# Kernel tuning notes

Hardware: AMD Instinct MI355X
Metric: run time of the kernel (lower is better)

The kernel has to match this reference:

```python
import jax, jax.numpy as jnp
import numpy as np

H = 100  # hidden size
EPS = 1e-5  # BatchNorm1d default eps


def setup_inputs() -> dict:
    key = jax.random.key(0)
    ks = jax.random.split(key, 9)
    s_ih = 1.0 / np.sqrt(H)
    inp = {
        "x": jax.random.normal(ks[0], (16, 4096, 40), dtype=jnp.float32),
        "W_ih": jax.random.uniform(ks[1], (4 * H, 40), jnp.float32, -s_ih, s_ih),
        "W_hh": jax.random.uniform(ks[2], (4 * H, H), jnp.float32, -s_ih, s_ih),
        "b_ih": jax.random.uniform(ks[3], (4 * H,), jnp.float32, -s_ih, s_ih),
        "b_hh": jax.random.uniform(ks[4], (4 * H,), jnp.float32, -s_ih, s_ih),
        "W1": jax.random.uniform(ks[5], (H, H), jnp.float32, -s_ih, s_ih),
        "b1": jax.random.uniform(ks[6], (H,), jnp.float32, -s_ih, s_ih),
        "gamma": jnp.ones((H,), jnp.float32),
        "beta": jnp.zeros((H,), jnp.float32),
        "W2": jax.random.uniform(ks[7], (40, H), jnp.float32, -s_ih, s_ih),
        "b2": jax.random.uniform(ks[8], (40,), jnp.float32, -s_ih, s_ih),
    }
    return inp


def _lstm_last_h(x, W_ih, W_hh, b_ih, b_hh):
    # x: [B, T, 40] -> precompute input projections for all timesteps
    B = x.shape[0]
    xg = jnp.einsum("bti,gi->tbg", x, W_ih) + b_ih + b_hh  # [T, B, 4H]
    W_hh_T = W_hh.T  # [H, 4H]

    def step(carry, xg_t):
        h, c = carry
        z = xg_t + h @ W_hh_T  # [B, 4H]
        i = jax.nn.sigmoid(z[:, 0 * H:1 * H])
        f = jax.nn.sigmoid(z[:, 1 * H:2 * H])
        g = jnp.tanh(z[:, 2 * H:3 * H])
        o = jax.nn.sigmoid(z[:, 3 * H:4 * H])
        c = f * c + i * g
        h = o * jnp.tanh(c)
        return (h, c), None

    h0 = jnp.zeros((B, H), x.dtype)
    c0 = jnp.zeros((B, H), x.dtype)
    (h_T, _), _ = jax.lax.scan(step, (h0, c0), xg)
    return h_T  # [B, H] == out[:, -1, :]


def reference(x, W_ih, W_hh, b_ih, b_hh, W1, b1, gamma, beta, W2, b2):
    h = _lstm_last_h(x, W_ih, W_hh, b_ih, b_hh)  # [B, H]
    y = h @ W1.T + b1  # Linear(100, 100)
    # BatchNorm1d in training mode: batch statistics, biased variance
    mu = jnp.mean(y, axis=0)
    var = jnp.mean((y - mu) ** 2, axis=0)
    y = (y - mu) * jax.lax.rsqrt(var + EPS) * gamma + beta
    y = y @ W2.T + b2  # Linear(100, 40)
    return y.reshape(-1, 10, 4)
```

## Files before the change

kernel.cpp:

```cpp
#include <hip/hip_runtime.h>
#include <cstddef>
#include <cstdint>

#define H100  100
#define G4    400
#define BATCH 16
#define TTOT  4096
#define NIN   40

__device__ __forceinline__ float fast_rcp(float x) { return __builtin_amdgcn_rcpf(x); }

__device__ __forceinline__ float gate_act(float z, bool is_g) {
    float m = is_g ? -2.0f : -1.0f;
    float e = __expf(m * z);
    float r = fast_rcp(1.0f + e);
    return is_g ? (2.0f * r - 1.0f) : r;
}
__device__ __forceinline__ float tanh_fast(float x) {
    float e = __expf(-2.0f * x);
    float r = fast_rcp(1.0f + e);
    return 2.0f * r - 1.0f;
}

__global__ __launch_bounds__(256) void xg_kernel(
    const float* __restrict__ x, const float* __restrict__ W_ih,
    const float* __restrict__ b_ih, const float* __restrict__ b_hh,
    float* __restrict__ xg, int t0, int steps, int chunkT)
{
    __shared__ float W_lds[NIN * G4];
    __shared__ float x_lds[16 * NIN];
    __shared__ float bias_lds[G4];

    int tid = threadIdx.x;
    int blocks_per_b = (steps + 15) >> 4;
    int b   = blockIdx.x / blocks_per_b;
    int tt  = blockIdx.x % blocks_per_b;
    int lt0 = tt * 16;
    int ntau = min(16, steps - lt0);

    for (int p = tid; p < NIN * G4; p += 256) {
        int g = p / NIN, i = p % NIN;
        W_lds[i * G4 + g] = W_ih[p];
    }
    for (int p = tid; p < G4; p += 256) bias_lds[p] = b_ih[p] + b_hh[p];
    const float* xsrc = x + ((size_t)b * TTOT + (size_t)(t0 + lt0)) * NIN;
    for (int p = tid; p < ntau * NIN; p += 256) x_lds[p] = xsrc[p];
    __syncthreads();

    int ntask = ntau * G4;
    for (int p = tid; p < ntask; p += 256) {
        int tau = p / G4, g = p % G4;
        float acc = bias_lds[g];
        #pragma unroll
        for (int i = 0; i < NIN; i++)
            acc = fmaf(x_lds[tau * NIN + i], W_lds[i * G4 + g], acc);
        xg[((size_t)b * chunkT + (size_t)(lt0 + tau)) * G4 + g] = acc;
    }
}

using h2_t = decltype(__builtin_amdgcn_cvt_pkrtz(0.0f, 0.0f));

__device__ __forceinline__ int h2i(h2_t v) { int r; __builtin_memcpy(&r, &v, 4); return r; }
__device__ __forceinline__ h2_t i2h(int v) { h2_t r; __builtin_memcpy(&r, &v, 4); return r; }

#if __has_builtin(__builtin_amdgcn_fdot2)
__device__ __forceinline__ float fdot2(h2_t a, h2_t b, float c) {
    return __builtin_amdgcn_fdot2(a, b, c, false);
}
#else
__device__ __forceinline__ float fdot2(h2_t a, h2_t b, float c) {
    float d;
    asm("v_dot2_f32_f16 %0, %1, %2, %3" : "=v"(d) : "v"(a), "v"(b), "v"(c));
    return d;
}
#endif

#define PIN1(a) asm volatile("" : "+v"(a))

__global__ __launch_bounds__(256)
__attribute__((amdgpu_waves_per_eu(1, 1)))
void lstm_kernel(
    const float* __restrict__ xg, const float* __restrict__ W_hh,
    float* __restrict__ hc, int t0, int steps, int chunkT)
{
    __shared__ float a_lds[2][G4];

    const int x = threadIdx.x;
    const int b = blockIdx.x;
    const int l = x & 63;
    const bool hasB = (x < G4 - 256);
    const int  rA = x;
    const int  rB = hasB ? (x + 256) : 0;

    const float2* wra2 = (const float2*)(W_hh + (size_t)rA * H100);
    const float2* wrb2 = (const float2*)(W_hh + (size_t)rB * H100);
#define LDW(q) \
    int wa##q = h2i(__builtin_amdgcn_cvt_pkrtz(wra2[q].x, wra2[q].y)); \
    int wb##q = h2i(__builtin_amdgcn_cvt_pkrtz(wrb2[q].x, wrb2[q].y)); \
    PIN1(wa##q); PIN1(wb##q);
    LDW(0)  LDW(1)  LDW(2)  LDW(3)  LDW(4)  LDW(5)  LDW(6)  LDW(7)
    LDW(8)  LDW(9)  LDW(10) LDW(11) LDW(12) LDW(13) LDW(14) LDW(15)
    LDW(16) LDW(17) LDW(18) LDW(19) LDW(20) LDW(21) LDW(22) LDW(23)
    LDW(24) LDW(25) LDW(26) LDW(27) LDW(28) LDW(29) LDW(30) LDW(31)
    LDW(32) LDW(33) LDW(34) LDW(35) LDW(36) LDW(37) LDW(38) LDW(39)
    LDW(40) LDW(41) LDW(42) LDW(43) LDW(44) LDW(45) LDW(46) LDW(47)
    LDW(48) LDW(49)
#undef LDW

    float* hch = hc;
    float* hcc = hc + BATCH * H100;

    float h0 = 0.f, h1 = 0.f, c0 = 0.f, c1 = 0.f;
    int hpi = 0;
    if (l < 50) {
        if (t0 != 0) {
            float2 hv = ((const float2*)(hch + b * H100))[l];
            float2 cv = ((const float2*)(hcc + b * H100))[l];
            h0 = hv.x; h1 = hv.y; c0 = cv.x; c1 = cv.y;
        }
        hpi = h2i(__builtin_amdgcn_cvt_pkrtz(h0, h1));
    }

    const float* xgb = xg + (size_t)b * chunkT * G4;
    float xcA = xgb[rA];
    float xcB = hasB ? xgb[rB] : 0.0f;

    const bool is_gA = (x >= 200) && (x < 300);
    const bool is_gB = (x < 44);

#define RLH2(src, idx) i2h(__builtin_amdgcn_readlane((src), (idx)))
#define DOTQ(q, aA, aB) { const h2_t u = RLH2(hpi, q); \
    aA = fdot2(i2h(wa##q), u, aA); \
    aB = fdot2(i2h(wb##q), u, aB); }

    #pragma unroll 1
    for (int t = 0; t < steps; t++) {
        float nxA = 0.f, nxB = 0.f;
        if (t + 1 < steps) {
            const float* p = xgb + (size_t)(t + 1) * G4;
            nxA = p[rA];
            nxB = p[rB];
        }

        float aA0 = 0, aA1 = 0, aB0 = 0, aB1 = 0;
        DOTQ(0,  aA0, aB0) DOTQ(1,  aA1, aB1) DOTQ(2,  aA0, aB0) DOTQ(3,  aA1, aB1)
        DOTQ(4,  aA0, aB0) DOTQ(5,  aA1, aB1) DOTQ(6,  aA0, aB0) DOTQ(7,  aA1, aB1)
        DOTQ(8,  aA0, aB0) DOTQ(9,  aA1, aB1) DOTQ(10, aA0, aB0) DOTQ(11, aA1, aB1)
        DOTQ(12, aA0, aB0) DOTQ(13, aA1, aB1) DOTQ(14, aA0, aB0) DOTQ(15, aA1, aB1)
        DOTQ(16, aA0, aB0) DOTQ(17, aA1, aB1) DOTQ(18, aA0, aB0) DOTQ(19, aA1, aB1)
        DOTQ(20, aA0, aB0) DOTQ(21, aA1, aB1) DOTQ(22, aA0, aB0) DOTQ(23, aA1, aB1)
        DOTQ(24, aA0, aB0) DOTQ(25, aA1, aB1) DOTQ(26, aA0, aB0) DOTQ(27, aA1, aB1)
        DOTQ(28, aA0, aB0) DOTQ(29, aA1, aB1) DOTQ(30, aA0, aB0) DOTQ(31, aA1, aB1)
        DOTQ(32, aA0, aB0) DOTQ(33, aA1, aB1) DOTQ(34, aA0, aB0) DOTQ(35, aA1, aB1)
        DOTQ(36, aA0, aB0) DOTQ(37, aA1, aB1) DOTQ(38, aA0, aB0) DOTQ(39, aA1, aB1)
        DOTQ(40, aA0, aB0) DOTQ(41, aA1, aB1) DOTQ(42, aA0, aB0) DOTQ(43, aA1, aB1)
        DOTQ(44, aA0, aB0) DOTQ(45, aA1, aB1) DOTQ(46, aA0, aB0) DOTQ(47, aA1, aB1)
        DOTQ(48, aA0, aB0) DOTQ(49, aA1, aB1)

        float zA = xcA + (aA0 + aA1);
        float zB = xcB + (aB0 + aB1);

        const int par = t & 1;
        a_lds[par][rA] = gate_act(zA, is_gA);
        if (hasB) a_lds[par][x + 256] = gate_act(zB, is_gB);
        asm volatile("s_waitcnt lgkmcnt(0)" ::: "memory");
        __builtin_amdgcn_s_barrier();

        if (l < 50) {
            const float* ab = a_lds[par];
            float2 gi = ((const float2*)(ab))[l];
            float2 gf = ((const float2*)(ab + 100))[l];
            float2 gg = ((const float2*)(ab + 200))[l];
            float2 go = ((const float2*)(ab + 300))[l];
            c0 = fmaf(gf.x, c0, gi.x * gg.x);
            c1 = fmaf(gf.y, c1, gi.y * gg.y);
            h0 = go.x * tanh_fast(c0);
            h1 = go.y * tanh_fast(c1);
            hpi = h2i(__builtin_amdgcn_cvt_pkrtz(h0, h1));
        }
        xcA = nxA; xcB = nxB;
    }

    if (x < 64 && l < 50) {
        ((float2*)(hch + b * H100))[l] = make_float2(h0, h1);
        ((float2*)(hcc + b * H100))[l] = make_float2(c0, c1);
    }
#undef DOTQ
#undef RLH2
}

__global__ __launch_bounds__(256) void head_kernel(
    const float* __restrict__ hc, const float* __restrict__ W1,
    const float* __restrict__ b1, const float* __restrict__ gamma,
    const float* __restrict__ beta, const float* __restrict__ W2,
    const float* __restrict__ b2, float* __restrict__ out)
{
    __shared__ float h_s[BATCH * H100];
    __shared__ float W1_s[H100 * 101];
    __shared__ float y1_s[BATCH * H100];
    __shared__ float W2_s[40 * 101];
    __shared__ float scale_s[H100], shift_s[H100];

    int tid = threadIdx.x;
    for (int p = tid; p < BATCH * H100; p += 256) h_s[p] = hc[p];
    for (int p = tid; p < H100 * H100; p += 256)
        W1_s[(p / H100) * 101 + p % H100] = W1[p];
    for (int p = tid; p < 40 * H100; p += 256)
        W2_s[(p / H100) * 101 + p % H100] = W2[p];
    __syncthreads();

    for (int p = tid; p < BATCH * H100; p += 256) {
        int b = p / H100, j = p % H100;
        float acc = b1[j];
        for (int k = 0; k < H100; k++)
            acc = fmaf(h_s[b * H100 + k], W1_s[j * 101 + k], acc);
        y1_s[b * H100 + j] = acc;
    }
    __syncthreads();

    if (tid < H100) {
        float mu = 0.0f;
        for (int b = 0; b < BATCH; b++) mu += y1_s[b * H100 + tid];
        mu *= (1.0f / BATCH);
        float var = 0.0f;
        for (int b = 0; b < BATCH; b++) {
            float d = y1_s[b * H100 + tid] - mu;
            var = fmaf(d, d, var);
        }
        var *= (1.0f / BATCH);
        float sc = gamma[tid] * rsqrtf(var + 1e-5f);
        scale_s[tid] = sc;
        shift_s[tid] = beta[tid] - mu * sc;
    }
    __syncthreads();

    for (int p = tid; p < BATCH * 40; p += 256) {
        int b = p / 40, o = p % 40;
        float acc = b2[o];
        for (int k = 0; k < H100; k++)
            acc = fmaf(fmaf(y1_s[b * H100 + k], scale_s[k], shift_s[k]),
                       W2_s[o * 101 + k], acc);
        out[p] = acc;
    }
}

extern "C" void kernel_launch(void* const* d_in, const int* in_sizes, int n_in,
                              void* d_out, int out_size, void* d_ws, size_t ws_size,
                              hipStream_t stream)
{
    const float* x     = (const float*)d_in[0];
    const float* W_ih  = (const float*)d_in[1];
    const float* W_hh  = (const float*)d_in[2];
    const float* b_ih  = (const float*)d_in[3];
    const float* b_hh  = (const float*)d_in[4];
    const float* W1    = (const float*)d_in[5];
    const float* b1    = (const float*)d_in[6];
    const float* gamma = (const float*)d_in[7];
    const float* beta  = (const float*)d_in[8];
    const float* W2    = (const float*)d_in[9];
    const float* b2    = (const float*)d_in[10];
    float* out = (float*)d_out;

    float* hc = (float*)d_ws;
    float* xg = (float*)((char*)d_ws + 16384);
    size_t avail    = ws_size > 16384 ? ws_size - 16384 : 0;
    size_t per_step = (size_t)BATCH * G4 * sizeof(float);
    size_t ct       = (avail / per_step) & ~(size_t)15;
    int chunkT = ct > TTOT ? TTOT : (int)ct;
    if (chunkT < 16) chunkT = 16;

    for (int t0 = 0; t0 < TTOT; t0 += chunkT) {
        int steps = (TTOT - t0 < chunkT) ? (TTOT - t0) : chunkT;
        int bpb = (steps + 15) / 16;
        xg_kernel<<<dim3(BATCH * bpb), 256, 0, stream>>>(
            x, W_ih, b_ih, b_hh, xg, t0, steps, chunkT);
        lstm_kernel<<<dim3(BATCH), 256, 0, stream>>>(
            xg, W_hh, hc, t0, steps, chunkT);
    }
    head_kernel<<<1, 256, 0, stream>>>(hc, W1, b1, gamma, beta, W2, b2, out);
}
```

Before: 2.727 ms.

## Store precomputed input projections in fp16 and enlarge xg time tile

The precomputed input-gate projections are now written and read as half precision, halving workspace traffic and letting larger chunks fit in the workspace, so fewer kernel launches may be needed. The xg kernel's time tile grows from 16 to 128 steps, so the W_ih transpose into LDS is amortised over more timesteps at the cost of fewer blocks. The recurrent kernel converts the halves back to float. The risk is precision loss in the gate pre-activations accumulated over 4096 steps, while the serial recurrence likely still dominates runtime.

```diff
diff --git a/kernel.cpp b/kernel.cpp
--- a/kernel.cpp
+++ b/kernel.cpp
@@ -1,4 +1,5 @@
 #include <hip/hip_runtime.h>
+#include <hip/hip_fp16.h>
 #include <cstddef>
 #include <cstdint>
 
@@ -7,6 +8,7 @@
 #define BATCH 16
 #define TTOT  4096
 #define NIN   40
+#define TAU   128
 
 __device__ __forceinline__ float fast_rcp(float x) { return __builtin_amdgcn_rcpf(x); }
 
@@ -25,18 +27,18 @@
 __global__ __launch_bounds__(256) void xg_kernel(
     const float* __restrict__ x, const float* __restrict__ W_ih,
     const float* __restrict__ b_ih, const float* __restrict__ b_hh,
-    float* __restrict__ xg, int t0, int steps, int chunkT)
+    __half* __restrict__ xg, int t0, int steps, int chunkT)
 {
     __shared__ float W_lds[NIN * G4];
-    __shared__ float x_lds[16 * NIN];
+    __shared__ float x_lds[TAU * NIN];
     __shared__ float bias_lds[G4];
 
     int tid = threadIdx.x;
-    int blocks_per_b = (steps + 15) >> 4;
+    int blocks_per_b = (steps + TAU - 1) / TAU;
     int b   = blockIdx.x / blocks_per_b;
     int tt  = blockIdx.x % blocks_per_b;
-    int lt0 = tt * 16;
-    int ntau = min(16, steps - lt0);
+    int lt0 = tt * TAU;
+    int ntau = min(TAU, steps - lt0);
 
     for (int p = tid; p < NIN * G4; p += 256) {
         int g = p / NIN, i = p % NIN;
@@ -54,7 +56,7 @@
         #pragma unroll
         for (int i = 0; i < NIN; i++)
             acc = fmaf(x_lds[tau * NIN + i], W_lds[i * G4 + g], acc);
-        xg[((size_t)b * chunkT + (size_t)(lt0 + tau)) * G4 + g] = acc;
+        xg[((size_t)b * chunkT + (size_t)(lt0 + tau)) * G4 + g] = __float2half(acc);
     }
 }
 
@@ -80,7 +82,7 @@
 __global__ __launch_bounds__(256)
 __attribute__((amdgpu_waves_per_eu(1, 1)))
 void lstm_kernel(
-    const float* __restrict__ xg, const float* __restrict__ W_hh,
+    const __half* __restrict__ xg, const float* __restrict__ W_hh,
     float* __restrict__ hc, int t0, int steps, int chunkT)
 {
     __shared__ float a_lds[2][G4];
@@ -121,9 +123,9 @@
         hpi = h2i(__builtin_amdgcn_cvt_pkrtz(h0, h1));
     }
 
-    const float* xgb = xg + (size_t)b * chunkT * G4;
-    float xcA = xgb[rA];
-    float xcB = hasB ? xgb[rB] : 0.0f;
+    const __half* xgb = xg + (size_t)b * chunkT * G4;
+    float xcA = __half2float(xgb[rA]);
+    float xcB = hasB ? __half2float(xgb[rB]) : 0.0f;
 
     const bool is_gA = (x >= 200) && (x < 300);
     const bool is_gB = (x < 44);
@@ -137,9 +139,9 @@
     for (int t = 0; t < steps; t++) {
         float nxA = 0.f, nxB = 0.f;
         if (t + 1 < steps) {
-            const float* p = xgb + (size_t)(t + 1) * G4;
-            nxA = p[rA];
-            nxB = p[rB];
+            const __half* p = xgb + (size_t)(t + 1) * G4;
+            nxA = __half2float(p[rA]);
+            nxB = __half2float(p[rB]);
         }
 
         float aA0 = 0, aA1 = 0, aB0 = 0, aB1 = 0;
@@ -261,17 +263,17 @@
     const float* b2    = (const float*)d_in[10];
     float* out = (float*)d_out;
 
-    float* hc = (float*)d_ws;
-    float* xg = (float*)((char*)d_ws + 16384);
+    float*  hc = (float*)d_ws;
+    __half* xg = (__half*)((char*)d_ws + 16384);
     size_t avail    = ws_size > 16384 ? ws_size - 16384 : 0;
-    size_t per_step = (size_t)BATCH * G4 * sizeof(float);
-    size_t ct       = (avail / per_step) & ~(size_t)15;
+    size_t per_step = (size_t)BATCH * G4 * sizeof(__half);
+    size_t ct       = (avail / per_step) & ~(size_t)(TAU - 1);
     int chunkT = ct > TTOT ? TTOT : (int)ct;
-    if (chunkT < 16) chunkT = 16;
+    if (chunkT < TAU) chunkT = TAU;
 
     for (int t0 = 0; t0 < TTOT; t0 += chunkT) {
         int steps = (TTOT - t0 < chunkT) ? (TTOT - t0) : chunkT;
-        int bpb = (steps + 15) / 16;
+        int bpb = (steps + TAU - 1) / TAU;
         xg_kernel<<<dim3(BATCH * bpb), 256, 0, stream>>>(
             x, W_ih, b_ih, b_hh, xg, t0, steps, chunkT);
         lstm_kernel<<<dim3(BATCH), 256, 0, stream>>>(
```

After: 3.472 ms. +27.3%, slower.
